# Kernel tuning notes

Hardware: AMD Instinct MI355X
Metric: run time of the kernel (lower is better)

Reference implementation:

```python
import math
import jax, jax.numpy as jnp
import numpy as np

D_MODEL = 1024
N_HEADS = 16
D_K = D_MODEL // N_HEADS
B = 8
L = 1024
LATTICE = (4, 4)
TWO_PI = 2.0 * math.pi


def _build_neighbors():
    """Replicates LatticeMultiHeadAttention._build_neighbors (Moore 8-neighborhood)."""
    positions = [divmod(i, LATTICE[1]) for i in range(N_HEADS)]
    idx = np.full((N_HEADS, 8), -1, dtype=np.int64)
    w = np.zeros((N_HEADS, 8), dtype=np.float32)
    for i, (r1, c1) in enumerate(positions):
        k = 0
        for dr in (-1, 0, 1):
            for dc in (-1, 0, 1):
                if dr == 0 and dc == 0:
                    continue
                if k >= 8:
                    break
                r2, c2 = r1 + dr, c1 + dc
                for j, (r, c) in enumerate(positions):
                    if (r, c) == (r2, c2):
                        idx[i, k] = j
                        w[i, k] = math.exp(-math.hypot(dr, dc))
                        k += 1
                        break
    return idx, w


def setup_inputs() -> dict:
    key = jax.random.key(0)
    ks = jax.random.split(key, 8)
    s = 1.0 / math.sqrt(D_MODEL)
    nbr_idx_np, nbr_w_np = _build_neighbors()
    return {
        "query": jax.random.normal(ks[0], (B, L, D_MODEL), jnp.float32),
        "key_": jax.random.normal(ks[1], (B, L, D_MODEL), jnp.float32),
        "value": jax.random.normal(ks[2], (B, L, D_MODEL), jnp.float32),
        # head-stacked projection weights, stored as [H, d_model, d_k] (x @ W)
        "Wq": jax.random.normal(ks[3], (N_HEADS, D_MODEL, D_K), jnp.float32) * s,
        "Wk": jax.random.normal(ks[4], (N_HEADS, D_MODEL, D_K), jnp.float32) * s,
        "Wv": jax.random.normal(ks[5], (N_HEADS, D_MODEL, D_K), jnp.float32) * s,
        "Wo": jax.random.normal(ks[6], (D_MODEL, D_MODEL), jnp.float32) * s,
        "bo": jax.random.normal(ks[7], (D_MODEL,), jnp.float32) * 0.01,
        # buffers: initial phases (0.0), intrinsic freqs 1 + 0.1*h, lattice tables
        "phases0": jnp.zeros((N_HEADS,), jnp.float32),
        "freqs": jnp.asarray(1.0 + 0.1 * np.arange(N_HEADS), jnp.float32),
        "nbr_w": jnp.asarray(nbr_w_np),
        "nbr_idx": jnp.asarray(nbr_idx_np),
    }


def _updated_phases(phases0, freqs, nbr_w, nbr_idx):
    # multi-head batched Kuramoto step (note: coupling_strength is NOT used here,
    # matching the original forward), then the per-head internal step (empty
    # neighbor_phases branch adds another 0.01 * intrinsic_freq).
    valid = (nbr_idx >= 0).astype(phases0.dtype)        # [H,8]
    nbr_ph = phases0[jnp.clip(nbr_idx, 0, None)] * valid  # [H,8]
    phase_diff = nbr_ph - phases0[:, None]
    force = (nbr_w * jnp.sin(phase_diff)).sum(axis=1)     # [H]
    p1 = jnp.mod(phases0 + 0.01 * (freqs + force), TWO_PI)
    p2 = jnp.mod(p1 + 0.01 * freqs, TWO_PI)
    return p2


def reference(query, key_, value, Wq, Wk, Wv, Wo, bo, phases0, freqs, nbr_w, nbr_idx):
    # phases are torch buffers updated under no_grad -> constants w.r.t. autodiff
    p2 = jax.lax.stop_gradient(
        _updated_phases(phases0, freqs, nbr_w, nbr_idx))
    bias = 0.1 * jnp.cos(p2)                               # [H]

    Q = jnp.einsum('bld,hdk->bhlk', query, Wq)
    K = jnp.einsum('bld,hdk->bhlk', key_, Wk)
    V = jnp.einsum('bld,hdk->bhlk', value, Wv)

    scores = jnp.einsum('bhlk,bhmk->bhlm', Q, K) / jnp.sqrt(
        jnp.asarray(D_K, Q.dtype))
    scores = scores + bias[None, :, None, None]
    attn = jax.nn.softmax(scores, axis=-1)                 # [B,H,L,L]
    ctx = jnp.einsum('bhlm,bhmk->bhlk', attn, V)           # [B,H,L,d_k]
    ctx = ctx.transpose(0, 2, 1, 3).reshape(query.shape[0], query.shape[1], D_MODEL)
    return ctx @ Wo + bo                                   # out_proj
```

## Files before the change

### kernel.cpp

```cpp
#include <hip/hip_runtime.h>
#include <hip/hip_bf16.h>
#include <stdint.h>


typedef unsigned short u16;
typedef __bf16 bf16_t;
typedef bf16_t bf16x8 __attribute__((ext_vector_type(8)));
typedef float f32x4 __attribute__((ext_vector_type(4)));

#define DEVI static __device__ __forceinline__
#define MFMA16(a, b, c) __builtin_amdgcn_mfma_f32_16x16x32_bf16((a), (b), (c), 0, 0, 0)

DEVI void gload_lds16(const void* g, void* l) {
  __builtin_amdgcn_global_load_lds((__attribute__((address_space(1))) void*)g,
                                   (__attribute__((address_space(3))) void*)l, 16, 0, 0);
}

DEVI u16 f2bf(float x) {
  bf16_t b = (bf16_t)x;
  u16 u;
  __builtin_memcpy(&u, &b, 2);
  return u;
}

__global__ __launch_bounds__(256) void prep(const float* __restrict__ Wq,
                                            const float* __restrict__ Wk,
                                            const float* __restrict__ Wv,
                                            const float* __restrict__ Wo,
                                            const float* __restrict__ q,
                                            const float* __restrict__ k,
                                            const float* __restrict__ v,
                                            u16* __restrict__ ws) {
  int bx = blockIdx.x;
  if (bx < 2048) {
    int id = bx * 256 + threadIdx.x;
    int mat = id >> 17;
    int rem = id & 131071;
    const float* src = (mat == 0) ? Wq : (mat == 1) ? Wk : (mat == 2) ? Wv : Wo;
    u16* dst = ws + (size_t)mat * 1048576;
    if (mat < 3) {
      int jb = rem & 7;
      int kk = (rem >> 3) & 1023;
      int h = rem >> 13;
      const float* s = src + h * 65536 + kk * 64 + jb * 8;
      float4 a = *(const float4*)s;
      float4 b = *(const float4*)(s + 4);
      float vv[8] = {a.x, a.y, a.z, a.w, b.x, b.y, b.z, b.w};
#pragma unroll
      for (int jj = 0; jj < 8; jj++)
        dst[(size_t)(h * 64 + jb * 8 + jj) * 1024 + kk] = f2bf(vv[jj]);
    } else {
      int cb = rem & 127;
      int d = rem >> 7;
      const float* s = src + d * 1024 + cb * 8;
      float4 a = *(const float4*)s;
      float4 b = *(const float4*)(s + 4);
      float vv[8] = {a.x, a.y, a.z, a.w, b.x, b.y, b.z, b.w};
#pragma unroll
      for (int jj = 0; jj < 8; jj++)
        dst[(size_t)(cb * 8 + jj) * 1024 + d] = f2bf(vv[jj]);
    }
  } else {
    int id = (bx - 2048) * 256 + threadIdx.x;
    int t = id >> 21;
    size_t rem = (size_t)(id & 2097151) * 4;
    const float* src = (t == 0) ? q : (t == 1) ? k : v;
    float4 a = *(const float4*)(src + rem);
    ushort4 st;
    st.x = f2bf(a.x); st.y = f2bf(a.y); st.z = f2bf(a.z); st.w = f2bf(a.w);
    *(ushort4*)(ws + 4194304 + (size_t)t * 8388608 + rem) = st;
  }
}

__global__ __launch_bounds__(256) void gemm_qkv(const u16* __restrict__ WT,
                                                const u16* __restrict__ X,
                                                u16* __restrict__ Qw,
                                                u16* __restrict__ Kw,
                                                u16* __restrict__ Vw) {
  __shared__ __align__(16) u16 sA[128 * 32];
  __shared__ __align__(16) u16 sB[128 * 32];
  int id = blockIdx.x + 8 * (blockIdx.y + 64 * blockIdx.z);
  int xcd = id & 7, j = id >> 3;
  int mtile = j & 7;
  int g = xcd * 24 + (j >> 3);
  int z = g >> 6;
  int nt = g & 63;
  const u16* A = WT + (size_t)z * 1048576;
  const u16* Bx = X + (size_t)z * 8388608;
  u16* out = (z == 0) ? Qw : (z == 1) ? Kw : Vw;
  float oscale = (z == 0) ? 0.125f : 1.0f;

  int tid = threadIdx.x;
  int wid = tid >> 6, lane = tid & 63, quad = lane >> 4, l16 = lane & 15;
  int wm = wid >> 1, wn = wid & 1;
  int m0 = mtile * 128, n0 = nt * 128;

  f32x4 acc[4][4];
#pragma unroll
  for (int i = 0; i < 4; i++)
#pragma unroll
    for (int jj = 0; jj < 4; jj++) acc[i][jj] = {0.f, 0.f, 0.f, 0.f};

  for (int k0 = 0; k0 < 1024; k0 += 32) {
#pragma unroll
    for (int p = 0; p < 2; p++) {
      int cl = p * 256 + tid;
      int r = cl >> 2, kc = cl & 3;
      gload_lds16(A + (size_t)(m0 + r) * 1024 + k0 + kc * 8,
                  (char*)sA + (p * 256 + wid * 64) * 16);
      gload_lds16(Bx + (size_t)(n0 + r) * 1024 + k0 + kc * 8,
                  (char*)sB + (p * 256 + wid * 64) * 16);
    }
    __syncthreads();
    bf16x8 af[4], bfr[4];
#pragma unroll
    for (int mt = 0; mt < 4; mt++)
      af[mt] = *(const bf16x8*)((const char*)sA + ((wm * 64 + mt * 16 + l16) * 64 + quad * 16));
#pragma unroll
    for (int ntf = 0; ntf < 4; ntf++)
      bfr[ntf] = *(const bf16x8*)((const char*)sB + ((wn * 64 + ntf * 16 + l16) * 64 + quad * 16));
#pragma unroll
    for (int mt = 0; mt < 4; mt++)
#pragma unroll
      for (int ntf = 0; ntf < 4; ntf++) acc[mt][ntf] = MFMA16(af[mt], bfr[ntf], acc[mt][ntf]);
    __syncthreads();
  }

#pragma unroll
  for (int mt = 0; mt < 4; mt++) {
    int m = m0 + wm * 64 + mt * 16 + quad * 4;
#pragma unroll
    for (int ntf = 0; ntf < 4; ntf++) {
      int n = n0 + wn * 64 + ntf * 16 + l16;
      f32x4 v = acc[mt][ntf];
      int b = n >> 10, l = n & 1023, h = m >> 6, dk = m & 63;
      if (z < 2) {
        ushort4 st;
        st.x = f2bf(v[0] * oscale); st.y = f2bf(v[1] * oscale);
        st.z = f2bf(v[2] * oscale); st.w = f2bf(v[3] * oscale);
        *(ushort4*)(out + ((size_t)((b * 16 + h) * 1024 + l) * 64 + dk)) = st;
      } else {
        size_t base = ((size_t)((b * 16 + h) * 64 + dk)) * 1024 + l;
        out[base] = f2bf(v[0]);
        out[base + 1024] = f2bf(v[1]);
        out[base + 2048] = f2bf(v[2]);
        out[base + 3072] = f2bf(v[3]);
      }
    }
  }
}

__global__ __launch_bounds__(256) void gemm_out(const u16* __restrict__ A,
                                                const u16* __restrict__ Bx,
                                                float* __restrict__ outf,
                                                const float* __restrict__ bias) {
  __shared__ __align__(16) u16 sA[128 * 32];
  __shared__ __align__(16) u16 sB[128 * 32];
  int id = blockIdx.x + 8 * blockIdx.y;
  int xcd = id & 7, j = id >> 3;
  int mtile = j & 7;
  int nt = xcd * 8 + (j >> 3);
  int tid = threadIdx.x;
  int wid = tid >> 6, lane = tid & 63, quad = lane >> 4, l16 = lane & 15;
  int wm = wid >> 1, wn = wid & 1;
  int m0 = mtile * 128, n0 = nt * 128;

  f32x4 acc[4][4];
#pragma unroll
  for (int i = 0; i < 4; i++)
#pragma unroll
    for (int jj = 0; jj < 4; jj++) acc[i][jj] = {0.f, 0.f, 0.f, 0.f};

  for (int k0 = 0; k0 < 1024; k0 += 32) {
#pragma unroll
    for (int p = 0; p < 2; p++) {
      int cl = p * 256 + tid;
      int r = cl >> 2, kc = cl & 3;
      gload_lds16(A + (size_t)(m0 + r) * 1024 + k0 + kc * 8,
                  (char*)sA + (p * 256 + wid * 64) * 16);
      gload_lds16(Bx + (size_t)(n0 + r) * 1024 + k0 + kc * 8,
                  (char*)sB + (p * 256 + wid * 64) * 16);
    }
    __syncthreads();
    bf16x8 af[4], bfr[4];
#pragma unroll
    for (int mt = 0; mt < 4; mt++)
      af[mt] = *(const bf16x8*)((const char*)sA + ((wm * 64 + mt * 16 + l16) * 64 + quad * 16));
#pragma unroll
    for (int ntf = 0; ntf < 4; ntf++)
      bfr[ntf] = *(const bf16x8*)((const char*)sB + ((wn * 64 + ntf * 16 + l16) * 64 + quad * 16));
#pragma unroll
    for (int mt = 0; mt < 4; mt++)
#pragma unroll
      for (int ntf = 0; ntf < 4; ntf++) acc[mt][ntf] = MFMA16(af[mt], bfr[ntf], acc[mt][ntf]);
    __syncthreads();
  }

#pragma unroll
  for (int mt = 0; mt < 4; mt++) {
    int m = m0 + wm * 64 + mt * 16 + quad * 4;
#pragma unroll
    for (int ntf = 0; ntf < 4; ntf++) {
      int n = n0 + wn * 64 + ntf * 16 + l16;
      f32x4 v = acc[mt][ntf];
      float4 st;
      st.x = v[0] + bias[m];
      st.y = v[1] + bias[m + 1];
      st.z = v[2] + bias[m + 2];
      st.w = v[3] + bias[m + 3];
      *(float4*)(outf + ((size_t)n * 1024 + m)) = st;
    }
  }
}

__global__ __launch_bounds__(256, 4) void attn_k(const u16* __restrict__ Q,
                                                 const u16* __restrict__ K,
                                                 const u16* __restrict__ VT,
                                                 u16* __restrict__ CTX) {
  __shared__ __align__(16) u16 sQ[128 * 64];
  __shared__ __align__(16) u16 sK[64 * 64];
  __shared__ __align__(16) u16 sV[64 * 64];
  int tid = threadIdx.x;
  int wid = tid >> 6, lane = tid & 63, quad = lane >> 4, l16 = lane & 15;
  int id = blockIdx.x + 8 * blockIdx.y;
  int xcd = id & 7, j = id >> 3;
  int qt = j & 7;
  int bh = xcd * 16 + (j >> 3);
  const u16* Qb = Q + (size_t)bh * 65536;
  const u16* Kb = K + (size_t)bh * 65536;
  const u16* Vb = VT + (size_t)bh * 65536;
  int q0 = qt * 128;

#pragma unroll
  for (int p = 0; p < 4; p++) {
    int cl = p * 256 + tid;
    int r = cl >> 3, c = cl & 7, g = c ^ (r & 7);
    gload_lds16(Qb + (size_t)(q0 + r) * 64 + g * 8, (char*)sQ + (p * 256 + wid * 64) * 16);
  }
  __syncthreads();

  bf16x8 bq[2][2];
#pragma unroll
  for (int qf = 0; qf < 2; qf++) {
    int row = wid * 32 + qf * 16 + l16;
#pragma unroll
    for (int ks = 0; ks < 2; ks++) {
      int ch = (ks * 4 + quad) ^ (row & 7);
      bq[qf][ks] = *(const bf16x8*)((const char*)sQ + row * 128 + ch * 16);
    }
  }

  u16* sPw = sQ + wid * 2048;

  f32x4 oacc[4][2];
#pragma unroll
  for (int i = 0; i < 4; i++) {
    oacc[i][0] = {0.f, 0.f, 0.f, 0.f};
    oacc[i][1] = {0.f, 0.f, 0.f, 0.f};
  }
  float lsum[2] = {0.f, 0.f};

  for (int lk0 = 0; lk0 < 1024; lk0 += 64) {
#pragma unroll
    for (int p = 0; p < 2; p++) {
      int cl = p * 256 + tid;
      int r = cl >> 3, c = cl & 7, g = c ^ (r & 7);
      gload_lds16(Kb + (size_t)(lk0 + r) * 64 + g * 8, (char*)sK + (p * 256 + wid * 64) * 16);
      gload_lds16(Vb + (size_t)r * 1024 + lk0 + g * 8, (char*)sV + (p * 256 + wid * 64) * 16);
    }
    __syncthreads();

    f32x4 s[4][2];
#pragma unroll
    for (int mt = 0; mt < 4; mt++) {
      s[mt][0] = {0.f, 0.f, 0.f, 0.f};
      s[mt][1] = {0.f, 0.f, 0.f, 0.f};
    }
#pragma unroll
    for (int ks = 0; ks < 2; ks++) {
#pragma unroll
      for (int mt = 0; mt < 4; mt++) {
        int row = mt * 16 + l16;
        int ch = (ks * 4 + quad) ^ (row & 7);
        bf16x8 a = *(const bf16x8*)((const char*)sK + row * 128 + ch * 16);
        s[mt][0] = MFMA16(a, bq[0][ks], s[mt][0]);
        s[mt][1] = MFMA16(a, bq[1][ks], s[mt][1]);
      }
    }

#pragma unroll
    for (int qf = 0; qf < 2; qf++) {
      int row = qf * 16 + l16;
#pragma unroll
      for (int mt = 0; mt < 4; mt++) {
        float p0 = __expf(s[mt][qf][0]);
        float p1 = __expf(s[mt][qf][1]);
        float p2 = __expf(s[mt][qf][2]);
        float p3 = __expf(s[mt][qf][3]);
        lsum[qf] += (p0 + p1) + (p2 + p3);
        ushort4 st;
        st.x = f2bf(p0); st.y = f2bf(p1); st.z = f2bf(p2); st.w = f2bf(p3);
        int ch = (2 * mt + (quad >> 1)) ^ (row & 7);
        *(ushort4*)((char*)sPw + row * 128 + ch * 16 + (quad & 1) * 8) = st;
      }
    }
    asm volatile("s_waitcnt lgkmcnt(0)" ::: "memory");

    bf16x8 bp[2][2];
#pragma unroll
    for (int qf = 0; qf < 2; qf++) {
      int row = qf * 16 + l16;
#pragma unroll
      for (int c = 0; c < 2; c++) {
        int ch = (c * 4 + quad) ^ (row & 7);
        bp[qf][c] = *(const bf16x8*)((const char*)sPw + row * 128 + ch * 16);
      }
    }
#pragma unroll
    for (int c = 0; c < 2; c++) {
#pragma unroll
      for (int mt = 0; mt < 4; mt++) {
        int row = mt * 16 + l16;
        int ch = (c * 4 + quad) ^ (row & 7);
        bf16x8 a = *(const bf16x8*)((const char*)sV + row * 128 + ch * 16);
        oacc[mt][0] = MFMA16(a, bp[0][c], oacc[mt][0]);
        oacc[mt][1] = MFMA16(a, bp[1][c], oacc[mt][1]);
      }
    }
    __syncthreads();
  }

#pragma unroll
  for (int qf = 0; qf < 2; qf++) {
    lsum[qf] += __shfl_xor(lsum[qf], 16, 64);
    lsum[qf] += __shfl_xor(lsum[qf], 32, 64);
  }
  float inv0 = 1.f / lsum[0], inv1 = 1.f / lsum[1];

  int b = bh >> 4, h = bh & 15;
#pragma unroll
  for (int qf = 0; qf < 2; qf++) {
    int qg = q0 + wid * 32 + qf * 16 + l16;
    float inv = qf ? inv1 : inv0;
#pragma unroll
    for (int mt = 0; mt < 4; mt++) {
      int dk = mt * 16 + quad * 4;
      ushort4 st;
      st.x = f2bf(oacc[mt][qf][0] * inv);
      st.y = f2bf(oacc[mt][qf][1] * inv);
      st.z = f2bf(oacc[mt][qf][2] * inv);
      st.w = f2bf(oacc[mt][qf][3] * inv);
      *(ushort4*)(CTX + (((size_t)(b * 1024 + qg) * 16 + h) * 64 + dk)) = st;
    }
  }
}

extern "C" void kernel_launch(void* const* d_in, const int* in_sizes, int n_in,
                              void* d_out, int out_size, void* d_ws, size_t ws_size,
                              hipStream_t stream) {
  (void)in_sizes; (void)n_in; (void)out_size;
  const float* query = (const float*)d_in[0];
  const float* key_ = (const float*)d_in[1];
  const float* value = (const float*)d_in[2];
  const float* Wq = (const float*)d_in[3];
  const float* Wk = (const float*)d_in[4];
  const float* Wv = (const float*)d_in[5];
  const float* Wo = (const float*)d_in[6];
  const float* bo = (const float*)d_in[7];

  u16* ws = (u16*)d_ws;
  u16* WT = ws;
  u16* X = ws + 4194304;
  u16* Qw = ws + 29360128;
  u16* Kw = ws + 37748736;
  u16* Vw = ws + 46137344;
  u16* Cw = X;
  float* outp = (float*)d_out;

  prep<<<26624, 256, 0, stream>>>(Wq, Wk, Wv, Wo, query, key_, value, ws);
  gemm_qkv<<<dim3(8, 64, 3), 256, 0, stream>>>(WT, X, Qw, Kw, Vw);
  attn_k<<<dim3(8, 128), 256, 0, stream>>>(Qw, Kw, Vw, Cw);
  gemm_out<<<dim3(8, 64), 256, 0, stream>>>(WT + 3145728, Cw, outp, bo);
}
```

Before: 308.2 us.

## Fuse fp32-to-bf16 activation conversion into QKV GEMM loads; rewrite weight prep

Activations are no longer converted to bf16 in a separate prep pass. The QKV GEMM now streams fp32 query/key/value tiles straight into XOR-swizzled LDS and converts them to bf16 when reading fragments. The weight transpose kernel is rewritten so each thread writes 16 contiguous bf16 values in wide stores. This removes a full read-write pass over about 100 MB of activations. The cost is twice the global and LDS traffic per B tile inside the GEMM, plus conversion instructions in its inner loop.

```diff
diff --git a/kernel.cpp b/kernel.cpp
--- a/kernel.cpp
+++ b/kernel.cpp
@@ -23,70 +23,61 @@
   return u;
 }
 
-__global__ __launch_bounds__(256) void prep(const float* __restrict__ Wq,
-                                            const float* __restrict__ Wk,
-                                            const float* __restrict__ Wv,
-                                            const float* __restrict__ Wo,
-                                            const float* __restrict__ q,
-                                            const float* __restrict__ k,
-                                            const float* __restrict__ v,
-                                            u16* __restrict__ ws) {
-  int bx = blockIdx.x;
-  if (bx < 2048) {
-    int id = bx * 256 + threadIdx.x;
-    int mat = id >> 17;
-    int rem = id & 131071;
-    const float* src = (mat == 0) ? Wq : (mat == 1) ? Wk : (mat == 2) ? Wv : Wo;
-    u16* dst = ws + (size_t)mat * 1048576;
-    if (mat < 3) {
-      int jb = rem & 7;
-      int kk = (rem >> 3) & 1023;
-      int h = rem >> 13;
-      const float* s = src + h * 65536 + kk * 64 + jb * 8;
-      float4 a = *(const float4*)s;
-      float4 b = *(const float4*)(s + 4);
-      float vv[8] = {a.x, a.y, a.z, a.w, b.x, b.y, b.z, b.w};
-#pragma unroll
-      for (int jj = 0; jj < 8; jj++)
-        dst[(size_t)(h * 64 + jb * 8 + jj) * 1024 + kk] = f2bf(vv[jj]);
-    } else {
-      int cb = rem & 127;
-      int d = rem >> 7;
-      const float* s = src + d * 1024 + cb * 8;
-      float4 a = *(const float4*)s;
-      float4 b = *(const float4*)(s + 4);
-      float vv[8] = {a.x, a.y, a.z, a.w, b.x, b.y, b.z, b.w};
-#pragma unroll
-      for (int jj = 0; jj < 8; jj++)
-        dst[(size_t)(cb * 8 + jj) * 1024 + d] = f2bf(vv[jj]);
-    }
+__global__ __launch_bounds__(256) void prep_w(const float* __restrict__ Wq,
+                                              const float* __restrict__ Wk,
+                                              const float* __restrict__ Wv,
+                                              const float* __restrict__ Wo,
+                                              u16* __restrict__ ws) {
+  int blk = blockIdx.x;
+  int mat = blk >> 8, t = blk & 255;
+  const float* src = (mat == 0) ? Wq : (mat == 1) ? Wk : (mat == 2) ? Wv : Wo;
+  u16* dst = ws + (size_t)mat * 1048576;
+  int j = threadIdx.x >> 2;
+  int c = threadIdx.x & 3;
+  const float* sp;
+  int stride, row, col0;
+  if (mat < 3) {
+    int h = t >> 4, kt = t & 15;
+    int k0 = kt * 64 + c * 16;
+    sp = src + h * 65536 + (size_t)k0 * 64 + j;
+    stride = 64;
+    row = h * 64 + j;
+    col0 = k0;
   } else {
-    int id = (bx - 2048) * 256 + threadIdx.x;
-    int t = id >> 21;
-    size_t rem = (size_t)(id & 2097151) * 4;
-    const float* src = (t == 0) ? q : (t == 1) ? k : v;
-    float4 a = *(const float4*)(src + rem);
-    ushort4 st;
-    st.x = f2bf(a.x); st.y = f2bf(a.y); st.z = f2bf(a.z); st.w = f2bf(a.w);
-    *(ushort4*)(ws + 4194304 + (size_t)t * 8388608 + rem) = st;
-  }
+    int ct = t >> 4, dt = t & 15;
+    int d0 = dt * 64 + c * 16;
+    sp = src + (size_t)d0 * 1024 + ct * 64 + j;
+    stride = 1024;
+    row = ct * 64 + j;
+    col0 = d0;
+  }
+  u16 v[16];
+#pragma unroll
+  for (int i = 0; i < 16; i++) v[i] = f2bf(sp[(size_t)i * stride]);
+  uint4 a, b2;
+  __builtin_memcpy(&a, v, 16);
+  __builtin_memcpy(&b2, v + 8, 16);
+  *(uint4*)(dst + (size_t)row * 1024 + col0) = a;
+  *(uint4*)(dst + (size_t)row * 1024 + col0 + 8) = b2;
 }
 
 __global__ __launch_bounds__(256) void gemm_qkv(const u16* __restrict__ WT,
-                                                const u16* __restrict__ X,
+                                                const float* __restrict__ Xq,
+                                                const float* __restrict__ Xk,
+                                                const float* __restrict__ Xv,
                                                 u16* __restrict__ Qw,
                                                 u16* __restrict__ Kw,
                                                 u16* __restrict__ Vw) {
   __shared__ __align__(16) u16 sA[128 * 32];
-  __shared__ __align__(16) u16 sB[128 * 32];
+  __shared__ __align__(16) float sB[128 * 32];
   int id = blockIdx.x + 8 * (blockIdx.y + 64 * blockIdx.z);
-  int xcd = id & 7, j = id >> 3;
-  int mtile = j & 7;
-  int g = xcd * 24 + (j >> 3);
+  int xcd = id & 7, jj = id >> 3;
+  int mtile = jj & 7;
+  int g = xcd * 24 + (jj >> 3);
   int z = g >> 6;
   int nt = g & 63;
   const u16* A = WT + (size_t)z * 1048576;
-  const u16* Bx = X + (size_t)z * 8388608;
+  const float* Bx = (z == 0) ? Xq : (z == 1) ? Xk : Xv;
   u16* out = (z == 0) ? Qw : (z == 1) ? Kw : Vw;
   float oscale = (z == 0) ? 0.125f : 1.0f;
 
@@ -99,7 +90,7 @@
 #pragma unroll
   for (int i = 0; i < 4; i++)
 #pragma unroll
-    for (int jj = 0; jj < 4; jj++) acc[i][jj] = {0.f, 0.f, 0.f, 0.f};
+    for (int j2 = 0; j2 < 4; j2++) acc[i][j2] = {0.f, 0.f, 0.f, 0.f};
 
   for (int k0 = 0; k0 < 1024; k0 += 32) {
 #pragma unroll
@@ -108,7 +99,12 @@
       int r = cl >> 2, kc = cl & 3;
       gload_lds16(A + (size_t)(m0 + r) * 1024 + k0 + kc * 8,
                   (char*)sA + (p * 256 + wid * 64) * 16);
-      gload_lds16(Bx + (size_t)(n0 + r) * 1024 + k0 + kc * 8,
+    }
+#pragma unroll
+    for (int p = 0; p < 4; p++) {
+      int cl = p * 256 + tid;
+      int r = cl >> 3, c = cl & 7, gg = c ^ (r & 7);
+      gload_lds16(Bx + (size_t)(n0 + r) * 1024 + k0 + gg * 4,
                   (char*)sB + (p * 256 + wid * 64) * 16);
     }
     __syncthreads();
@@ -117,8 +113,20 @@
     for (int mt = 0; mt < 4; mt++)
       af[mt] = *(const bf16x8*)((const char*)sA + ((wm * 64 + mt * 16 + l16) * 64 + quad * 16));
 #pragma unroll
-    for (int ntf = 0; ntf < 4; ntf++)
-      bfr[ntf] = *(const bf16x8*)((const char*)sB + ((wn * 64 + ntf * 16 + l16) * 64 + quad * 16));
+    for (int ntf = 0; ntf < 4; ntf++) {
+      int row = wn * 64 + ntf * 16 + l16;
+      const char* rp = (const char*)sB + row * 128;
+      int c0 = (quad * 2) ^ (row & 7);
+      int c1 = (quad * 2 + 1) ^ (row & 7);
+      f32x4 x0 = *(const f32x4*)(rp + c0 * 16);
+      f32x4 x1 = *(const f32x4*)(rp + c1 * 16);
+      bf16x8 f;
+      f[0] = (bf16_t)x0[0]; f[1] = (bf16_t)x0[1];
+      f[2] = (bf16_t)x0[2]; f[3] = (bf16_t)x0[3];
+      f[4] = (bf16_t)x1[0]; f[5] = (bf16_t)x1[1];
+      f[6] = (bf16_t)x1[2]; f[7] = (bf16_t)x1[3];
+      bfr[ntf] = f;
+    }
 #pragma unroll
     for (int mt = 0; mt < 4; mt++)
 #pragma unroll
@@ -358,7 +366,7 @@
 extern "C" void kernel_launch(void* const* d_in, const int* in_sizes, int n_in,
                               void* d_out, int out_size, void* d_ws, size_t ws_size,
                               hipStream_t stream) {
-  (void)in_sizes; (void)n_in; (void)out_size;
+  (void)in_sizes; (void)n_in; (void)out_size; (void)ws_size;
   const float* query = (const float*)d_in[0];
   const float* key_ = (const float*)d_in[1];
   const float* value = (const float*)d_in[2];
@@ -370,15 +378,14 @@
 
   u16* ws = (u16*)d_ws;
   u16* WT = ws;
-  u16* X = ws + 4194304;
-  u16* Qw = ws + 29360128;
-  u16* Kw = ws + 37748736;
-  u16* Vw = ws + 46137344;
-  u16* Cw = X;
+  u16* Qw = ws + 4194304;
+  u16* Kw = ws + 12582912;
+  u16* Vw = ws + 20971520;
+  u16* Cw = ws + 29360128;
   float* outp = (float*)d_out;
 
-  prep<<<26624, 256, 0, stream>>>(Wq, Wk, Wv, Wo, query, key_, value, ws);
-  gemm_qkv<<<dim3(8, 64, 3), 256, 0, stream>>>(WT, X, Qw, Kw, Vw);
+  prep_w<<<1024, 256, 0, stream>>>(Wq, Wk, Wv, Wo, ws);
+  gemm_qkv<<<dim3(8, 64, 3), 256, 0, stream>>>(WT, query, key_, value, Qw, Kw, Vw);
   attn_k<<<dim3(8, 128), 256, 0, stream>>>(Qw, Kw, Vw, Cw);
   gemm_out<<<dim3(8, 64), 256, 0, stream>>>(WT + 3145728, Cw, outp, bo);
 }
```

New measurement: 340.4 us. +10.5%, slower.
